# Kernel tuning notes

Measured on AMD Instinct MI355X. Metric: run time of the kernel, lower is better.

Reference implementation:

```python
import jax, jax.numpy as jnp
import numpy as np

BATCH = 1      # a
SEQ = 512      # b == h == num_query
DIM = 128      # c
N_HEADS = BATCH * SEQ  # n = 512, required by the module's view(n, c, h) contract


def setup_inputs() -> dict:
    key = jax.random.key(0)
    ks = jax.random.split(key, 9)
    s = 0.02  # small init scale for weights
    shp = (BATCH, SEQ, SEQ, DIM)
    return {
        "query": jax.random.normal(ks[0], shp, jnp.float32),
        "key": jax.random.normal(ks[1], shp, jnp.float32),
        "value": jax.random.normal(ks[2], shp, jnp.float32),
        "Wq": jax.random.normal(ks[3], (DIM, DIM), jnp.float32) * s,
        "bq": jax.random.normal(ks[4], (DIM,), jnp.float32) * s,
        "Wk": jax.random.normal(ks[5], (DIM, DIM), jnp.float32) * s,
        "bk": jax.random.normal(ks[6], (DIM,), jnp.float32) * s,
        "Wv": jax.random.normal(ks[7], (DIM, DIM), jnp.float32) * s,
        "bv": jax.random.normal(ks[8], (DIM,), jnp.float32) * s,
    }


def reference(query, key, value, Wq, bq, Wk, bk, Wv, bv):
    n, c = N_HEADS, DIM
    h = query.shape[1]  # SEQ

    def proj(x, W, b):
        # torch Linear: x @ W.T + b, then view(n, c, h).transpose(-2,-1).unsqueeze(1)
        y = x @ W.T + b                       # (a, b, b, c)
        y = y.reshape(n, c, h)                # row-major reshape, same as torch .view
        return jnp.swapaxes(y, -2, -1)[:, None]  # (n, 1, h, c)

    q = proj(query, Wq, bq)
    k = proj(key, Wk, bk)
    v = proj(value, Wv, bv)

    attn = (q @ jnp.swapaxes(k, -1, -2)) / jnp.sqrt(jnp.float32(c))  # (n,1,h,h)
    attn = jax.nn.softmax(attn, axis=-1)
    # dropout p=0.66 is identity in eval mode
    ctxt = (attn @ v)[:, 0]  # (n, h, c)

    batch_size, num_query = query.shape[0], query.shape[1]
    output = ctxt.reshape(batch_size, num_query, h * c)  # (a, b, b*c)
    return output, attn
```

## Files before the change

kernel.cpp:

```cpp
#include <hip/hip_runtime.h>
#include <stdint.h>

typedef float f32x4 __attribute__((ext_vector_type(4)));
typedef short s16x8 __attribute__((ext_vector_type(8)));
typedef short s16x4 __attribute__((ext_vector_type(4)));

#define MFMA16(a, b, c) __builtin_amdgcn_mfma_f32_16x16x32_bf16(a, b, c, 0, 0, 0)

__device__ __forceinline__ unsigned short f2bf(float f) {
  union { float f; uint32_t u; } v; v.f = f;
  return (unsigned short)((v.u + 0x7FFFu + ((v.u >> 16) & 1u)) >> 16);
}
__device__ __forceinline__ float bf2f(unsigned short s) {
  union { float f; uint32_t u; } v; v.u = ((uint32_t)s) << 16;
  return v.f;
}
__device__ __forceinline__ s16x8 cvt8(const float* p) {
  f32x4 a = *(const f32x4*)p;
  f32x4 b = *(const f32x4*)(p + 4);
  s16x8 t;
  t[0] = (short)f2bf(a[0]); t[1] = (short)f2bf(a[1]);
  t[2] = (short)f2bf(a[2]); t[3] = (short)f2bf(a[3]);
  t[4] = (short)f2bf(b[0]); t[5] = (short)f2bf(b[1]);
  t[6] = (short)f2bf(b[2]); t[7] = (short)f2bf(b[3]);
  return t;
}
template <int N> __device__ __forceinline__ void vmwait() {
  asm volatile("s_waitcnt vmcnt(%0)" ::"i"(N) : "memory");
}
__device__ __forceinline__ void blockbar() {
  __builtin_amdgcn_s_barrier();
  asm volatile("" ::: "memory");
}
__device__ __forceinline__ void gl_lds16(const void* g, void* l) {
  __builtin_amdgcn_global_load_lds((const __attribute__((address_space(1))) void*)g,
                                   (__attribute__((address_space(3))) void*)l, 16, 0, 0);
}

__global__ __launch_bounds__(256) void proj_kernel(
    const float* __restrict__ Xq, const float* __restrict__ Xk, const float* __restrict__ Xv,
    const float* __restrict__ Wq, const float* __restrict__ bq,
    const float* __restrict__ Wk, const float* __restrict__ bk,
    const float* __restrict__ Wv, const float* __restrict__ bv,
    unsigned short* __restrict__ Qt, unsigned short* __restrict__ Kt,
    unsigned short* __restrict__ Vf) {
  __shared__ unsigned char Wsh[32768];

  const int ty = blockIdx.y;
  const float* X = (ty == 0) ? Xq : (ty == 1) ? Xk : Xv;
  const float* W = (ty == 0) ? Wq : (ty == 1) ? Wk : Wv;
  const float* B = (ty == 0) ? bq : (ty == 1) ? bk : bv;
  unsigned short* out = (ty == 0) ? Qt : (ty == 1) ? Kt : Vf;
  const bool transposed = (ty != 2);

  const int tid = threadIdx.x;
  const int lane = tid & 63;
  const int wave = tid >> 6;
  const int l15 = lane & 15;
  const int g = lane >> 4;

  {
    const int r = tid >> 1;
    const int cb = (tid & 1) * 64;
    const float* wp = W + (size_t)r * 128 + cb;
#pragma unroll
    for (int c8 = 0; c8 < 8; ++c8) {
      s16x8 w = cvt8(wp + 8 * c8);
      const int byte = r * 256 + ((cb * 2 + c8 * 16) ^ ((r & 7) << 4));
      *(s16x8*)(Wsh + byte) = w;
    }
  }
  __syncthreads();

  auto wfrag = [&](int f, int kc) -> s16x8 {
    const int row = 16 * f + l15;
    return *(const s16x8*)(Wsh + row * 256 + ((64 * kc + 16 * g) ^ ((row & 7) << 4)));
  };

  if (transposed) {
    float bias_s[8];
#pragma unroll
    for (int f = 0; f < 8; ++f) bias_s[f] = B[16 * f + l15];

    auto loadX = [&](s16x8 (&xf)[4], int t) {
      const int jb = blockIdx.x * 512 + t * 64 + wave * 16;
      const int jrow = jb + (l15 >> 2) + 4 * (l15 & 3);
      const float* xr = X + (size_t)jrow * 128 + 8 * g;
#pragma unroll
      for (int kc = 0; kc < 4; ++kc) xf[kc] = cvt8(xr + 32 * kc);
    };
    auto storeT = [&](f32x4 (&acc)[8], int t) {
      const int jb = blockIdx.x * 512 + t * 64 + wave * 16;
      const int n = jb >> 9;
      const int c0 = (jb & 511) >> 2;
#pragma unroll
      for (int f = 0; f < 8; ++f) {
        const int h = 128 * g + 16 * f + l15;
        s16x4 pv;
#pragma unroll
        for (int r = 0; r < 4; ++r) pv[r] = (short)f2bf(acc[f][r] + bias_s[f]);
        *(s16x4*)(out + (size_t)n * 65536 + (size_t)h * 128 + c0) = pv;
      }
    };
    auto computePair = [&](s16x8 (&x0)[4], s16x8 (&x1)[4], int t0) {
      f32x4 accA[8], accB[8];
#pragma unroll
      for (int f = 0; f < 8; ++f) {
        accA[f] = (f32x4){0.f, 0.f, 0.f, 0.f};
        accB[f] = (f32x4){0.f, 0.f, 0.f, 0.f};
      }
#pragma unroll
      for (int kc = 0; kc < 4; ++kc)
#pragma unroll
        for (int f = 0; f < 8; ++f) {
          const s16x8 w = wfrag(f, kc);
          accA[f] = MFMA16(x0[kc], w, accA[f]);
          accB[f] = MFMA16(x1[kc], w, accB[f]);
        }
      storeT(accA, t0);
      storeT(accB, t0 + 1);
    };

    s16x8 xA0[4], xA1[4], xB0[4], xB1[4];
    loadX(xA0, 0); loadX(xA1, 1);
#pragma unroll
    for (int tp = 0; tp < 8; tp += 2) {
      if ((tp & 2) == 0) {
        if (tp < 6) { loadX(xB0, tp + 2); loadX(xB1, tp + 3); }
        computePair(xA0, xA1, tp);
      } else {
        if (tp < 6) { loadX(xA0, tp + 2); loadX(xA1, tp + 3); }
        computePair(xB0, xB1, tp);
      }
    }
  } else {
    f32x4 bias_v[8];
#pragma unroll
    for (int f = 0; f < 8; ++f) bias_v[f] = *(const f32x4*)(B + 16 * f + 4 * g);

    auto loadX = [&](s16x8 (&xf)[4], int t) {
      const int jb = blockIdx.x * 512 + t * 64 + wave * 16;
      const int jrow = jb + l15;
      const float* xr = X + (size_t)jrow * 128 + 8 * g;
#pragma unroll
      for (int kc = 0; kc < 4; ++kc) xf[kc] = cvt8(xr + 32 * kc);
    };
    auto storeV = [&](f32x4 (&acc)[8], int t) {
      const int jb = blockIdx.x * 512 + t * 64 + wave * 16;
      const int j = jb + l15;
#pragma unroll
      for (int f = 0; f < 8; ++f) {
        const int cc0 = 16 * f + 4 * g;
        s16x4 pv;
#pragma unroll
        for (int r = 0; r < 4; ++r) pv[r] = (short)f2bf(acc[f][r] + bias_v[f][r]);
        *(s16x4*)(out + (size_t)j * 128 + cc0) = pv;
      }
    };
    auto computePair = [&](s16x8 (&x0)[4], s16x8 (&x1)[4], int t0) {
      f32x4 accA[8], accB[8];
#pragma unroll
      for (int f = 0; f < 8; ++f) {
        accA[f] = (f32x4){0.f, 0.f, 0.f, 0.f};
        accB[f] = (f32x4){0.f, 0.f, 0.f, 0.f};
      }
#pragma unroll
      for (int kc = 0; kc < 4; ++kc)
#pragma unroll
        for (int f = 0; f < 8; ++f) {
          const s16x8 w = wfrag(f, kc);
          accA[f] = MFMA16(w, x0[kc], accA[f]);
          accB[f] = MFMA16(w, x1[kc], accB[f]);
        }
      storeV(accA, t0);
      storeV(accB, t0 + 1);
    };

    s16x8 xA0[4], xA1[4], xB0[4], xB1[4];
    loadX(xA0, 0); loadX(xA1, 1);
#pragma unroll
    for (int tp = 0; tp < 8; tp += 2) {
      if ((tp & 2) == 0) {
        if (tp < 6) { loadX(xB0, tp + 2); loadX(xB1, tp + 3); }
        computePair(xA0, xA1, tp);
      } else {
        if (tp < 6) { loadX(xA0, tp + 2); loadX(xA1, tp + 3); }
        computePair(xB0, xB1, tp);
      }
    }
  }
}

__global__ __launch_bounds__(512, 1) void fattn_kernel(
    const unsigned short* __restrict__ Qt, const unsigned short* __restrict__ Kt,
    const unsigned short* __restrict__ Vf, float* __restrict__ out0,
    float* __restrict__ attn_out) {
  __shared__ unsigned char Stg[32768];

  const int tid = threadIdx.x;
  const int lane = tid & 63;
  const int wave = tid >> 6;
  const int l15 = lane & 15;
  const int g = lane >> 4;

  const int bid = blockIdx.x;
  const int nb = (bid & 7) * 256 + (bid >> 3);
  const int head = nb >> 2;
  const int h0 = (nb & 3) * 128;
  const float scale = 0.08838834764831845f;

  const size_t khead = (size_t)head * 65536;
  const unsigned short* qbase =
      Qt + khead + (size_t)(h0 + 16 * wave + l15) * 128 + 8 * g;
  s16x8 qf0 = *(const s16x8*)(qbase);
  s16x8 qf1 = *(const s16x8*)(qbase + 32);
  s16x8 qf2 = *(const s16x8*)(qbase + 64);
  s16x8 qf3 = *(const s16x8*)(qbase + 96);

  const int sig = 8 * (l15 >> 2) + (l15 & 3);
  const unsigned short* Kh = Kt + khead;
  const unsigned short* Vh = Vf + khead;

  auto stageK = [&](int w) {
    const int i = wave;
    const int cl = i >> 2, kc = i & 3;
    const unsigned short* src =
        Kh + (size_t)sig * 128 + 8 * g + (size_t)w * 4096 + cl * 512 + 32 * kc;
    gl_lds16(src, Stg + (w & 3) * 8192 + i * 1024);
  };
  auto stageV = [&](int w) {
    const int i = wave;
    const int half = i >> 2, fi = i & 3;
    const unsigned short* src =
        Vh + (size_t)l15 * 512 + 8 * g + half * 32768 + w * 32 + (size_t)fi * 8192;
    gl_lds16(src, Stg + (w & 3) * 8192 + i * 1024);
  };

  const int lb = lane * 16;
  s16x8 st0, st1, st2, st3, st4, st5, st6, st7;
  s16x8 st8, st9, st10, st11, st12, st13, st14, st15;
  float rs = 0.f;

#define WINDOW_A(W, ST)                                              \
  do {                                                               \
    const unsigned char* kb8 = Stg + ((W) & 3) * 8192;               \
    s16x8 ka0 = *(const s16x8*)(kb8 + lb);                           \
    s16x8 ka1 = *(const s16x8*)(kb8 + 1024 + lb);                    \
    s16x8 ka2 = *(const s16x8*)(kb8 + 2048 + lb);                    \
    s16x8 ka3 = *(const s16x8*)(kb8 + 3072 + lb);                    \
    s16x8 kb0 = *(const s16x8*)(kb8 + 4096 + lb);                    \
    s16x8 kb1 = *(const s16x8*)(kb8 + 5120 + lb);                    \
    s16x8 kb2 = *(const s16x8*)(kb8 + 6144 + lb);                    \
    s16x8 kb3 = *(const s16x8*)(kb8 + 7168 + lb);                    \
    f32x4 sA = {0.f, 0.f, 0.f, 0.f}, sB = {0.f, 0.f, 0.f, 0.f};      \
    sA = MFMA16(ka0, qf0, sA); sA = MFMA16(ka1, qf1, sA);            \
    sA = MFMA16(ka2, qf2, sA); sA = MFMA16(ka3, qf3, sA);            \
    sB = MFMA16(kb0, qf0, sB); sB = MFMA16(kb1, qf1, sB);            \
    sB = MFMA16(kb2, qf2, sB); sB = MFMA16(kb3, qf3, sB);            \
    s16x8 fr;                                                        \
    float e;                                                         \
    e = __expf(sA[0] * scale); rs += e; fr[0] = (short)f2bf(e);      \
    e = __expf(sA[1] * scale); rs += e; fr[1] = (short)f2bf(e);      \
    e = __expf(sA[2] * scale); rs += e; fr[2] = (short)f2bf(e);      \
    e = __expf(sA[3] * scale); rs += e; fr[3] = (short)f2bf(e);      \
    e = __expf(sB[0] * scale); rs += e; fr[4] = (short)f2bf(e);      \
    e = __expf(sB[1] * scale); rs += e; fr[5] = (short)f2bf(e);      \
    e = __expf(sB[2] * scale); rs += e; fr[6] = (short)f2bf(e);      \
    e = __expf(sB[3] * scale); rs += e; fr[7] = (short)f2bf(e);      \
    ST = fr;                                                         \
  } while (0)

#define STEPA(W, ST)                                                 \
  do { vmwait<2>(); blockbar(); stageK((W) + 3); WINDOW_A(W, ST); } while (0)

  stageK(0); stageK(1); stageK(2);
  STEPA(0, st0);  STEPA(1, st1);  STEPA(2, st2);  STEPA(3, st3);
  STEPA(4, st4);  STEPA(5, st5);  STEPA(6, st6);  STEPA(7, st7);
  STEPA(8, st8);  STEPA(9, st9);  STEPA(10, st10); STEPA(11, st11);
  STEPA(12, st12);
  vmwait<2>(); blockbar(); WINDOW_A(13, st13);
  vmwait<1>(); blockbar(); WINDOW_A(14, st14);
  vmwait<0>(); blockbar(); WINDOW_A(15, st15);

  rs += __shfl_xor(rs, 16);
  rs += __shfl_xor(rs, 32);
  const float inv = 1.0f / rs;

  blockbar();

  f32x4 acc2[8];
#pragma unroll
  for (int f = 0; f < 8; ++f) acc2[f] = (f32x4){0.f, 0.f, 0.f, 0.f};

#define WINDOW_B(W, ST)                                                    \
  do {                                                                     \
    const s16x8 pc = ST;                                                   \
    const unsigned char* vb8 = Stg + ((W) & 3) * 8192;                     \
    acc2[0] = MFMA16(pc, *(const s16x8*)(vb8 + lb), acc2[0]);              \
    acc2[1] = MFMA16(pc, *(const s16x8*)(vb8 + 1024 + lb), acc2[1]);       \
    acc2[2] = MFMA16(pc, *(const s16x8*)(vb8 + 2048 + lb), acc2[2]);       \
    acc2[3] = MFMA16(pc, *(const s16x8*)(vb8 + 3072 + lb), acc2[3]);       \
    acc2[4] = MFMA16(pc, *(const s16x8*)(vb8 + 4096 + lb), acc2[4]);       \
    acc2[5] = MFMA16(pc, *(const s16x8*)(vb8 + 5120 + lb), acc2[5]);       \
    acc2[6] = MFMA16(pc, *(const s16x8*)(vb8 + 6144 + lb), acc2[6]);       \
    acc2[7] = MFMA16(pc, *(const s16x8*)(vb8 + 7168 + lb), acc2[7]);       \
  } while (0)

#define STEPB(W, ST)                                                 \
  do { vmwait<2>(); blockbar(); stageV((W) + 3); WINDOW_B(W, ST); } while (0)

  stageV(0); stageV(1); stageV(2);
  STEPB(0, st0);  STEPB(1, st1);  STEPB(2, st2);  STEPB(3, st3);
  STEPB(4, st4);  STEPB(5, st5);  STEPB(6, st6);  STEPB(7, st7);
  STEPB(8, st8);  STEPB(9, st9);  STEPB(10, st10); STEPB(11, st11);
  STEPB(12, st12);
  vmwait<2>(); blockbar(); WINDOW_B(13, st13);
  vmwait<1>(); blockbar(); WINDOW_B(14, st14);
  vmwait<0>(); blockbar(); WINDOW_B(15, st15);

  float* ap = attn_out + (size_t)head * 262144 + (size_t)(h0 + 16 * wave + l15) * 512 + 8 * g;

#define OUTW(W, ST)                                                  \
  do {                                                               \
    const s16x8 pc = ST;                                             \
    f32x4 o0, o1;                                                    \
    o0[0] = bf2f((unsigned short)pc[0]) * inv;                       \
    o0[1] = bf2f((unsigned short)pc[1]) * inv;                       \
    o0[2] = bf2f((unsigned short)pc[2]) * inv;                       \
    o0[3] = bf2f((unsigned short)pc[3]) * inv;                       \
    o1[0] = bf2f((unsigned short)pc[4]) * inv;                       \
    o1[1] = bf2f((unsigned short)pc[5]) * inv;                       \
    o1[2] = bf2f((unsigned short)pc[6]) * inv;                       \
    o1[3] = bf2f((unsigned short)pc[7]) * inv;                       \
    *(f32x4*)(ap + (W) * 32) = o0;                                   \
    *(f32x4*)(ap + (W) * 32 + 4) = o1;                               \
  } while (0)

  OUTW(0, st0);  OUTW(1, st1);  OUTW(2, st2);  OUTW(3, st3);
  OUTW(4, st4);  OUTW(5, st5);  OUTW(6, st6);  OUTW(7, st7);
  OUTW(8, st8);  OUTW(9, st9);  OUTW(10, st10); OUTW(11, st11);
  OUTW(12, st12); OUTW(13, st13); OUTW(14, st14); OUTW(15, st15);

  float invm[4];
#pragma unroll
  for (int r = 0; r < 4; ++r) invm[r] = __shfl(inv, 4 * g + r);

  float* op = out0 + khead + (size_t)(h0 + 16 * wave + 4 * g) * 128 + l15;
#pragma unroll
  for (int f = 0; f < 8; ++f)
#pragma unroll
    for (int r = 0; r < 4; ++r)
      __builtin_nontemporal_store(acc2[f][r] * invm[r], op + (size_t)r * 128 + f * 16);
}

extern "C" void kernel_launch(void* const* d_in, const int* in_sizes, int n_in,
                              void* d_out, int out_size, void* d_ws, size_t ws_size,
                              hipStream_t stream) {
  const float* q  = (const float*)d_in[0];
  const float* k  = (const float*)d_in[1];
  const float* v  = (const float*)d_in[2];
  const float* Wq = (const float*)d_in[3];
  const float* bq = (const float*)d_in[4];
  const float* Wk = (const float*)d_in[5];
  const float* bk = (const float*)d_in[6];
  const float* Wv = (const float*)d_in[7];
  const float* bv = (const float*)d_in[8];

  unsigned short* Qt = (unsigned short*)d_ws;
  unsigned short* Kt = Qt + 33554432;
  unsigned short* Vf = Kt + 33554432;
  float* out0 = (float*)d_out;
  float* attn = out0 + 33554432;

  dim3 pgrid(512, 3, 1);
  proj_kernel<<<pgrid, 256, 0, stream>>>(q, k, v, Wq, bq, Wk, bk, Wv, bv, Qt, Kt, Vf);
  fattn_kernel<<<2048, 512, 0, stream>>>(Qt, Kt, Vf, out0, attn);
}
```

Measured before the change: 467.7 us.

## Fuse Q projection into attention kernel, dropping Q workspace round-trip

Moves the Q linear projection out of the projection kernel into the attention kernel. Each attention block loads Wq into shared memory, computes its 128x128 Q tile with MFMA from fp32 inputs, and stages it in a new shared buffer before loading fragments. This removes the bf16 Q write and read through global memory and one third of the projection grid. In exchange it adds shared memory per block, two extra barriers and redundant Wq conversion in every one of the 2048 blocks.

```diff
diff --git a/kernel.cpp b/kernel.cpp
--- a/kernel.cpp
+++ b/kernel.cpp
@@ -38,20 +38,18 @@
 }
 
 __global__ __launch_bounds__(256) void proj_kernel(
-    const float* __restrict__ Xq, const float* __restrict__ Xk, const float* __restrict__ Xv,
-    const float* __restrict__ Wq, const float* __restrict__ bq,
+    const float* __restrict__ Xk, const float* __restrict__ Xv,
     const float* __restrict__ Wk, const float* __restrict__ bk,
     const float* __restrict__ Wv, const float* __restrict__ bv,
-    unsigned short* __restrict__ Qt, unsigned short* __restrict__ Kt,
-    unsigned short* __restrict__ Vf) {
+    unsigned short* __restrict__ Kt, unsigned short* __restrict__ Vf) {
   __shared__ unsigned char Wsh[32768];
 
   const int ty = blockIdx.y;
-  const float* X = (ty == 0) ? Xq : (ty == 1) ? Xk : Xv;
-  const float* W = (ty == 0) ? Wq : (ty == 1) ? Wk : Wv;
-  const float* B = (ty == 0) ? bq : (ty == 1) ? bk : bv;
-  unsigned short* out = (ty == 0) ? Qt : (ty == 1) ? Kt : Vf;
-  const bool transposed = (ty != 2);
+  const float* X = (ty == 0) ? Xk : Xv;
+  const float* W = (ty == 0) ? Wk : Wv;
+  const float* B = (ty == 0) ? bk : bv;
+  unsigned short* out = (ty == 0) ? Kt : Vf;
+  const bool transposed = (ty == 0);
 
   const int tid = threadIdx.x;
   const int lane = tid & 63;
@@ -192,10 +190,12 @@
 }
 
 __global__ __launch_bounds__(512, 1) void fattn_kernel(
-    const unsigned short* __restrict__ Qt, const unsigned short* __restrict__ Kt,
-    const unsigned short* __restrict__ Vf, float* __restrict__ out0,
-    float* __restrict__ attn_out) {
+    const float* __restrict__ Xq, const float* __restrict__ Wq,
+    const float* __restrict__ bq,
+    const unsigned short* __restrict__ Kt, const unsigned short* __restrict__ Vf,
+    float* __restrict__ out0, float* __restrict__ attn_out) {
   __shared__ unsigned char Stg[32768];
+  __shared__ unsigned char Qsh[32768];
 
   const int tid = threadIdx.x;
   const int lane = tid & 63;
@@ -209,14 +209,63 @@
   const int h0 = (nb & 3) * 128;
   const float scale = 0.08838834764831845f;
 
+  {
+    const int r = tid >> 2;
+    const int cb2 = (tid & 3) * 32;
+    const float* wp = Wq + (size_t)r * 128 + cb2;
+#pragma unroll
+    for (int c8 = 0; c8 < 4; ++c8) {
+      s16x8 w = cvt8(wp + 8 * c8);
+      const int byte = r * 256 + ((cb2 * 2 + c8 * 16) ^ ((r & 7) << 4));
+      *(s16x8*)(Stg + byte) = w;
+    }
+  }
+  __syncthreads();
+
+  {
+    auto wfrag = [&](int f, int kc) -> s16x8 {
+      const int row = 16 * f + l15;
+      return *(const s16x8*)(Stg + row * 256 + ((64 * kc + 16 * g) ^ ((row & 7) << 4)));
+    };
+    const int q4 = nb & 3;
+    const int jrow = 512 * head + 64 * wave + 4 * l15 + q4;
+    const float* xr = Xq + (size_t)jrow * 128 + 8 * g;
+    s16x8 xf[4];
+#pragma unroll
+    for (int kc = 0; kc < 4; ++kc) xf[kc] = cvt8(xr + 32 * kc);
+
+    float bias_s[8];
+#pragma unroll
+    for (int f = 0; f < 8; ++f) bias_s[f] = bq[16 * f + l15];
+
+    f32x4 acc[8];
+#pragma unroll
+    for (int f = 0; f < 8; ++f) acc[f] = (f32x4){0.f, 0.f, 0.f, 0.f};
+#pragma unroll
+    for (int kc = 0; kc < 4; ++kc)
+#pragma unroll
+      for (int f = 0; f < 8; ++f) acc[f] = MFMA16(xf[kc], wfrag(f, kc), acc[f]);
+
+    const int c0 = 16 * wave + 4 * g;
+#pragma unroll
+    for (int f = 0; f < 8; ++f) {
+      const int h = 16 * f + l15;
+      s16x4 pv;
+#pragma unroll
+      for (int r = 0; r < 4; ++r) pv[r] = (short)f2bf(acc[f][r] + bias_s[f]);
+      *(s16x4*)(Qsh + h * 256 + ((c0 * 2) ^ ((h & 7) << 4))) = pv;
+    }
+  }
+  __syncthreads();
+
+  const int hq = 16 * wave + l15;
+  const int qsw = (hq & 7) << 4;
+  s16x8 qf0 = *(const s16x8*)(Qsh + hq * 256 + ((0 + 16 * g) ^ qsw));
+  s16x8 qf1 = *(const s16x8*)(Qsh + hq * 256 + ((64 + 16 * g) ^ qsw));
+  s16x8 qf2 = *(const s16x8*)(Qsh + hq * 256 + ((128 + 16 * g) ^ qsw));
+  s16x8 qf3 = *(const s16x8*)(Qsh + hq * 256 + ((192 + 16 * g) ^ qsw));
+
   const size_t khead = (size_t)head * 65536;
-  const unsigned short* qbase =
-      Qt + khead + (size_t)(h0 + 16 * wave + l15) * 128 + 8 * g;
-  s16x8 qf0 = *(const s16x8*)(qbase);
-  s16x8 qf1 = *(const s16x8*)(qbase + 32);
-  s16x8 qf2 = *(const s16x8*)(qbase + 64);
-  s16x8 qf3 = *(const s16x8*)(qbase + 96);
-
   const int sig = 8 * (l15 >> 2) + (l15 & 3);
   const unsigned short* Kh = Kt + khead;
   const unsigned short* Vh = Vf + khead;
@@ -372,7 +421,7 @@
   float* out0 = (float*)d_out;
   float* attn = out0 + 33554432;
 
-  dim3 pgrid(512, 3, 1);
-  proj_kernel<<<pgrid, 256, 0, stream>>>(q, k, v, Wq, bq, Wk, bk, Wv, bv, Qt, Kt, Vf);
-  fattn_kernel<<<2048, 512, 0, stream>>>(Qt, Kt, Vf, out0, attn);
-}
+  dim3 pgrid(512, 2, 1);
+  proj_kernel<<<pgrid, 256, 0, stream>>>(k, v, Wk, bk, Wv, bv, Kt, Vf);
+  fattn_kernel<<<2048, 512, 0, stream>>>(q, Wq, bq, Kt, Vf, out0, attn);
+}
```

Result: no change. 461.3 us (-1.4%).
